# Optimization experiments

Measured on AMD Instinct MI355X. Metric: run time of the kernel, lower is better.

The kernel has to match this reference:

```python
import jax, jax.numpy as jnp
import numpy as np


def _resize_bilinear_ac(x, oh, ow):
    """Bilinear resize with align_corners=True for NCHW input."""
    ih, iw = x.shape[-2], x.shape[-1]
    ys = jnp.linspace(0.0, ih - 1.0, oh)
    xs = jnp.linspace(0.0, iw - 1.0, ow)
    y0 = jnp.floor(ys).astype(jnp.int32)
    y1 = jnp.minimum(y0 + 1, ih - 1)
    wy = (ys - y0).astype(x.dtype)[None, None, :, None]
    x0 = jnp.floor(xs).astype(jnp.int32)
    x1 = jnp.minimum(x0 + 1, iw - 1)
    wx = (xs - x0).astype(x.dtype)[None, None, None, :]
    top = x[:, :, y0, :] * (1 - wy) + x[:, :, y1, :] * wy  # (B,1,oh,iw)
    return top[:, :, :, x0] * (1 - wx) + top[:, :, :, x1] * wx  # (B,1,oh,ow)


def raw_to_rgb_bg(image):
    """Demosaic a (*,1,H,W) bayer raw image, CFA.BG layout (top-left red)."""
    orig_shape = image.shape
    H, W = image.shape[-2], image.shape[-1]
    img = image.reshape(-1, 1, H, W)

    # CFA.BG: red at even rows/cols, blue at odd rows/cols
    r = img[:, :, ::2, ::2]   # (B,1,H/2,W/2)
    b = img[:, :, 1::2, 1::2]
    # rpad=(0,1,0,1): pad right/bottom by 1; bpad=(1,0,1,0): pad left/top by 1 (replicate)
    rpadded = jnp.pad(r, ((0, 0), (0, 0), (0, 1), (0, 1)), mode='edge')
    bpadded = jnp.pad(b, ((0, 0), (0, 0), (1, 0), (1, 0)), mode='edge')

    ru = _resize_bilinear_ac(rpadded, H + 1, W + 1)
    bu = _resize_bilinear_ac(bpadded, H + 1, W + 1)
    # negative padding = crop back to (H, W)
    ru = ru[:, :, :H, :W]      # crop right/bottom
    bu = bu[:, :, 1:, 1:]      # crop left/top

    # green: reflect-pad and apply fixed cross kernel (4-neighbour average)
    gp = jnp.pad(img, ((0, 0), (0, 0), (1, 1), (1, 1)), mode='reflect')
    gu = 0.25 * (gp[:, :, :-2, 1:-1] + gp[:, :, 2:, 1:-1]
                 + gp[:, :, 1:-1, :-2] + gp[:, :, 1:-1, 2:])
    # overwrite known green samples (CFA.BG: green at (even,odd) and (odd,even))
    gu = gu.at[:, :, ::2, 1::2].set(img[:, :, ::2, 1::2])
    gu = gu.at[:, :, 1::2, ::2].set(img[:, :, 1::2, ::2])

    ru = ru.reshape(orig_shape)
    gu = gu.reshape(orig_shape)
    bu = bu.reshape(orig_shape)
    return jnp.concatenate([ru, gu, bu], axis=-3)


def setup_inputs() -> dict:
    key = jax.random.key(0)
    image = jax.random.uniform(key, (8, 1, 2048, 2048), dtype=jnp.float32)
    return {"image": image}


def reference(image):
    return raw_to_rgb_bg(image)
```

## Files before the change

### kernel.cpp

```cpp
#include <hip/hip_runtime.h>


#define HH 2048
#define WW 2048

__device__ __forceinline__ float ldx(const float* __restrict__ img, int y, int x) {
    return img[(size_t)y * WW + x];
}

__global__ __launch_bounds__(256) void demosaic_bg_kernel(const float* __restrict__ in,
                                                          float* __restrict__ out) {
    const int strips_per_row = WW / 4;
    int gid = blockIdx.x * blockDim.x + threadIdx.x;
    int s = gid & (strips_per_row - 1);
    int t = gid >> 9;
    int y = t & (HH - 1);
    int b = t >> 11;
    int x0 = s << 2;

    const float* __restrict__ img = in + (size_t)b * HH * WW;

    float R[4], G[4], B[4];
    const int py = y & 1;

    if (py == 0) {
        const int ym = (y == 0) ? 1 : y - 1;
        const int yp = y + 1;
#pragma unroll
        for (int i = 0; i < 4; ++i) {
            int x = x0 + i;
            if ((x & 1) == 0) {
                int xm = (x == 0) ? 1 : x - 1;
                int xp = x + 1;
                float c  = ldx(img, y, x);
                float u  = ldx(img, ym, x);
                float d  = ldx(img, yp, x);
                float l  = ldx(img, y, xm);
                float r  = ldx(img, y, xp);
                R[i] = c;
                G[i] = 0.25f * (u + d + l + r);
                B[i] = 0.25f * (ldx(img, ym, xm) + ldx(img, ym, xp) +
                                ldx(img, yp, xm) + ldx(img, yp, xp));
            } else {
                int xc = (x + 1 > WW - 2) ? (WW - 2) : x + 1;
                R[i] = 0.5f * (ldx(img, y, x - 1) + ldx(img, y, xc));
                G[i] = ldx(img, y, x);
                B[i] = 0.5f * (ldx(img, ym, x) + ldx(img, yp, x));
            }
        }
    } else {
        const int ycR = (y + 1 > HH - 2) ? (HH - 2) : y + 1;
        const int ymG = y - 1;
        const int ypG = (y == HH - 1) ? (HH - 2) : y + 1;
#pragma unroll
        for (int i = 0; i < 4; ++i) {
            int x = x0 + i;
            if ((x & 1) == 0) {
                int xm = (x == 0) ? 1 : x - 1;
                R[i] = 0.5f * (ldx(img, y - 1, x) + ldx(img, ycR, x));
                G[i] = ldx(img, y, x);
                B[i] = 0.5f * (ldx(img, y, xm) + ldx(img, y, x + 1));
            } else {
                int xcR = (x + 1 > WW - 2) ? (WW - 2) : x + 1;
                int xpG = (x == WW - 1) ? (WW - 2) : x + 1;
                R[i] = 0.25f * (ldx(img, y - 1, x - 1) + ldx(img, y - 1, xcR) +
                                ldx(img, ycR,  x - 1) + ldx(img, ycR,  xcR));
                G[i] = 0.25f * (ldx(img, ymG, x) + ldx(img, ypG, x) +
                                ldx(img, y, x - 1) + ldx(img, y, xpG));
                B[i] = ldx(img, y, x);
            }
        }
    }

    size_t obase = ((size_t)b * 3) * HH * WW + (size_t)y * WW + x0;
    float4* outR = (float4*)(out + obase);
    float4* outG = (float4*)(out + obase + (size_t)HH * WW);
    float4* outB = (float4*)(out + obase + 2 * (size_t)HH * WW);
    *outR = make_float4(R[0], R[1], R[2], R[3]);
    *outG = make_float4(G[0], G[1], G[2], G[3]);
    *outB = make_float4(B[0], B[1], B[2], B[3]);
}

extern "C" void kernel_launch(void* const* d_in, const int* in_sizes, int n_in,
                              void* d_out, int out_size, void* d_ws, size_t ws_size,
                              hipStream_t stream) {
    const float* in = (const float*)d_in[0];
    float* out = (float*)d_out;
    const int strips = 8 * HH * (WW / 4);
    dim3 block(256);
    dim3 grid(strips / 256);
    demosaic_bg_kernel<<<grid, block, 0, stream>>>(in, out);
}
```

Baseline: 499.9 us.

## Process two rows per thread with vectorized row loads for demosaic

Each thread now handles a 2x4 tile (an even and an odd row) instead of a single 1x4 strip. It loads four neighbouring rows once as float4 plus scalar left/right halos and computes all R/G/B values from registers. The many scalar global loads and the per-parity branching are replaced by a few vector loads shared across both rows. This halves the thread count and raises per-thread register use, which may lower occupancy on a bandwidth-bound kernel.

```diff
diff --git a/kernel.cpp b/kernel.cpp
--- a/kernel.cpp
+++ b/kernel.cpp
@@ -4,8 +4,16 @@
 #define HH 2048
 #define WW 2048
 
-__device__ __forceinline__ float ldx(const float* __restrict__ img, int y, int x) {
-    return img[(size_t)y * WW + x];
+struct Row { float l; float4 c; float r; };
+
+__device__ __forceinline__ Row load_row(const float* __restrict__ p, int x0) {
+    Row o;
+    int xl = (x0 == 0) ? 1 : x0 - 1;
+    int xr = (x0 + 4 > WW - 2) ? (WW - 2) : x0 + 4;
+    o.l = p[xl];
+    o.c = *(const float4*)(p + x0);
+    o.r = p[xr];
+    return o;
 }
 
 __global__ __launch_bounds__(256) void demosaic_bg_kernel(const float* __restrict__ in,
@@ -14,71 +22,63 @@
     int gid = blockIdx.x * blockDim.x + threadIdx.x;
     int s = gid & (strips_per_row - 1);
     int t = gid >> 9;
-    int y = t & (HH - 1);
-    int b = t >> 11;
+    int yp = t & (HH / 2 - 1);
+    int b = t >> 10;
+    int y = yp << 1;
     int x0 = s << 2;
 
     const float* __restrict__ img = in + (size_t)b * HH * WW;
 
-    float R[4], G[4], B[4];
-    const int py = y & 1;
+    const int i0 = (y == 0) ? 1 : y - 1;
+    const int i3 = (y + 2 > HH - 2) ? (HH - 2) : y + 2;
 
-    if (py == 0) {
-        const int ym = (y == 0) ? 1 : y - 1;
-        const int yp = y + 1;
-#pragma unroll
-        for (int i = 0; i < 4; ++i) {
-            int x = x0 + i;
-            if ((x & 1) == 0) {
-                int xm = (x == 0) ? 1 : x - 1;
-                int xp = x + 1;
-                float c  = ldx(img, y, x);
-                float u  = ldx(img, ym, x);
-                float d  = ldx(img, yp, x);
-                float l  = ldx(img, y, xm);
-                float r  = ldx(img, y, xp);
-                R[i] = c;
-                G[i] = 0.25f * (u + d + l + r);
-                B[i] = 0.25f * (ldx(img, ym, xm) + ldx(img, ym, xp) +
-                                ldx(img, yp, xm) + ldx(img, yp, xp));
-            } else {
-                int xc = (x + 1 > WW - 2) ? (WW - 2) : x + 1;
-                R[i] = 0.5f * (ldx(img, y, x - 1) + ldx(img, y, xc));
-                G[i] = ldx(img, y, x);
-                B[i] = 0.5f * (ldx(img, ym, x) + ldx(img, yp, x));
-            }
-        }
-    } else {
-        const int ycR = (y + 1 > HH - 2) ? (HH - 2) : y + 1;
-        const int ymG = y - 1;
-        const int ypG = (y == HH - 1) ? (HH - 2) : y + 1;
-#pragma unroll
-        for (int i = 0; i < 4; ++i) {
-            int x = x0 + i;
-            if ((x & 1) == 0) {
-                int xm = (x == 0) ? 1 : x - 1;
-                R[i] = 0.5f * (ldx(img, y - 1, x) + ldx(img, ycR, x));
-                G[i] = ldx(img, y, x);
-                B[i] = 0.5f * (ldx(img, y, xm) + ldx(img, y, x + 1));
-            } else {
-                int xcR = (x + 1 > WW - 2) ? (WW - 2) : x + 1;
-                int xpG = (x == WW - 1) ? (WW - 2) : x + 1;
-                R[i] = 0.25f * (ldx(img, y - 1, x - 1) + ldx(img, y - 1, xcR) +
-                                ldx(img, ycR,  x - 1) + ldx(img, ycR,  xcR));
-                G[i] = 0.25f * (ldx(img, ymG, x) + ldx(img, ypG, x) +
-                                ldx(img, y, x - 1) + ldx(img, y, xpG));
-                B[i] = ldx(img, y, x);
-            }
-        }
-    }
+    Row r0 = load_row(img + (size_t)i0 * WW, x0);
+    Row r1 = load_row(img + (size_t)y * WW, x0);
+    Row r2 = load_row(img + (size_t)(y + 1) * WW, x0);
+    Row r3 = load_row(img + (size_t)i3 * WW, x0);
 
-    size_t obase = ((size_t)b * 3) * HH * WW + (size_t)y * WW + x0;
-    float4* outR = (float4*)(out + obase);
-    float4* outG = (float4*)(out + obase + (size_t)HH * WW);
-    float4* outB = (float4*)(out + obase + 2 * (size_t)HH * WW);
-    *outR = make_float4(R[0], R[1], R[2], R[3]);
-    *outG = make_float4(G[0], G[1], G[2], G[3]);
-    *outB = make_float4(B[0], B[1], B[2], B[3]);
+    float4 Re, Ge, Be;
+    Re.x = r1.c.x;
+    Ge.x = 0.25f * (r0.c.x + r2.c.x + r1.l + r1.c.y);
+    Be.x = 0.25f * (r0.l + r0.c.y + r2.l + r2.c.y);
+
+    Re.y = 0.5f * (r1.c.x + r1.c.z);
+    Ge.y = r1.c.y;
+    Be.y = 0.5f * (r0.c.y + r2.c.y);
+
+    Re.z = r1.c.z;
+    Ge.z = 0.25f * (r0.c.z + r2.c.z + r1.c.y + r1.c.w);
+    Be.z = 0.25f * (r0.c.y + r0.c.w + r2.c.y + r2.c.w);
+
+    Re.w = 0.5f * (r1.c.z + r1.r);
+    Ge.w = r1.c.w;
+    Be.w = 0.5f * (r0.c.w + r2.c.w);
+
+    float4 Ro, Go, Bo;
+    Ro.x = 0.5f * (r1.c.x + r3.c.x);
+    Go.x = r2.c.x;
+    Bo.x = 0.5f * (r2.l + r2.c.y);
+
+    Ro.y = 0.25f * (r1.c.x + r1.c.z + r3.c.x + r3.c.z);
+    Go.y = 0.25f * (r1.c.y + r3.c.y + r2.c.x + r2.c.z);
+    Bo.y = r2.c.y;
+
+    Ro.z = 0.5f * (r1.c.z + r3.c.z);
+    Go.z = r2.c.z;
+    Bo.z = 0.5f * (r2.c.y + r2.c.w);
+
+    Ro.w = 0.25f * (r1.c.z + r1.r + r3.c.z + r3.r);
+    Go.w = 0.25f * (r1.c.w + r3.c.w + r2.c.z + r2.r);
+    Bo.w = r2.c.w;
+
+    const size_t plane = (size_t)HH * WW;
+    size_t obase = (size_t)b * 3 * plane + (size_t)y * WW + x0;
+    *(float4*)(out + obase)                 = Re;
+    *(float4*)(out + obase + WW)            = Ro;
+    *(float4*)(out + obase + plane)         = Ge;
+    *(float4*)(out + obase + plane + WW)    = Go;
+    *(float4*)(out + obase + 2 * plane)     = Be;
+    *(float4*)(out + obase + 2 * plane + WW) = Bo;
 }
 
 extern "C" void kernel_launch(void* const* d_in, const int* in_sizes, int n_in,
@@ -86,8 +86,8 @@
                               hipStream_t stream) {
     const float* in = (const float*)d_in[0];
     float* out = (float*)d_out;
-    const int strips = 8 * HH * (WW / 4);
+    const int threads = 8 * (HH / 2) * (WW / 4);
     dim3 block(256);
-    dim3 grid(strips / 256);
+    dim3 grid(threads / 256);
     demosaic_bg_kernel<<<grid, block, 0, stream>>>(in, out);
 }
```

After: 476.4 us. -4.7%, faster.
